# Kernel optimization log

Measured on AMD Instinct MI355X. Metric: run time of the kernel, lower is better.

## Reference

```python
import jax, jax.numpy as jnp
import numpy as np

DIM = 4096
R = 128
B, S = 4, 4096


def setup_inputs() -> dict:
    key = jax.random.key(0)
    k1, k2, k3 = jax.random.split(key, 3)
    x = jax.random.normal(k1, (B, S, DIM), dtype=jnp.float32)
    # PyTorch Linear default init: U(-1/sqrt(fan_in), 1/sqrt(fan_in)); approx with scaled normal
    W_down = jax.random.normal(k2, (R, DIM), dtype=jnp.float32) * (1.0 / np.sqrt(DIM))
    W_up = jax.random.normal(k3, (DIM, R), dtype=jnp.float32) * (1.0 / np.sqrt(R))
    return {"x": x, "W_down": W_down, "W_up": W_up}


def reference(x, W_down, W_up):
    # RMSNorm (no learned scale, eps = finfo(dtype).eps as in F.rms_norm default)
    eps = jnp.finfo(x.dtype).eps
    ms = jnp.mean(jnp.square(x), axis=-1, keepdims=True)
    xn = x * jax.lax.rsqrt(ms + eps)
    # low-rank gate: sigmoid(W_up @ silu(W_down @ xn))
    h = jax.nn.silu(jnp.einsum('bsd,rd->bsr', xn, W_down))  # [B,S,R]
    gate = jax.nn.sigmoid(jnp.einsum('bsr,dr->bsd', h, W_up))  # [B,S,DIM]
    return xn * gate
```

## Files before the change

kernel.cpp:

```cpp
#include <hip/hip_runtime.h>
#include <hip/hip_bf16.h>


#define DIMX  4096
#define RLOW  128
#define BT    16
#define THREADS 256

typedef __attribute__((ext_vector_type(8))) short  bf16x8;
typedef __attribute__((ext_vector_type(4))) float  f32x4;

__device__ __forceinline__ unsigned short f2bf(float f) {
    unsigned int u = __float_as_uint(f);
    u = u + 0x7fffu + ((u >> 16) & 1u);
    return (unsigned short)(u >> 16);
}
__device__ __forceinline__ float bf2f(unsigned short s) {
    return __uint_as_float((unsigned int)s << 16);
}
__device__ __forceinline__ float sigm(float v) { return 1.0f / (1.0f + __expf(-v)); }

__device__ __forceinline__ void cvt8_store(unsigned short* dst, float4 a, float4 b) {
    ushort4 u0, u1;
    u0.x = f2bf(a.x); u0.y = f2bf(a.y); u0.z = f2bf(a.z); u0.w = f2bf(a.w);
    u1.x = f2bf(b.x); u1.y = f2bf(b.y); u1.z = f2bf(b.z); u1.w = f2bf(b.w);
    *(ushort4*)dst = u0;
    *(ushort4*)(dst + 4) = u1;
}

__global__ __launch_bounds__(THREADS)
void prep_weights_frag(const float* __restrict__ wd, const float* __restrict__ wu,
                       unsigned short* __restrict__ wd_frag,
                       unsigned short* __restrict__ wu_frag) {
    const int tg = blockIdx.x * THREADS + threadIdx.x;
    if (tg < 65536) {
        const int frag = tg >> 6, lane = tg & 63;
        const int wave = frag & 3, nt = (frag >> 2) & 1, ks = (frag >> 3) & 7, c = frag >> 6;
        const int r = wave * 32 + nt * 16 + (lane & 15);
        const int k = c * 256 + ks * 32 + 8 * (lane >> 4);
        const float* src = wd + (long)r * DIMX + k;
        cvt8_store(wd_frag + ((long)frag << 9) + lane * 8,
                   *(const float4*)src, *(const float4*)(src + 4));
    } else {
        const int t2 = tg - 65536;
        const int frag = t2 >> 6, lane = t2 & 63;
        const int d_tile = frag >> 2, ks = frag & 3;
        const int row = d_tile * 16 + (lane & 15);
        const int col = ks * 32 + 8 * (lane >> 4);
        const float* src = wu + (long)row * RLOW + col;
        cvt8_store(wu_frag + ((long)frag << 9) + lane * 8,
                   *(const float4*)src, *(const float4*)(src + 4));
    }
}

#define KC        256
#define NCH       (DIMX / KC)
#define XB_STRIDE 8192
#define INV1_OFF  (2 * XB_STRIDE)
#define LDS1_BYTES (INV1_OFF + BT * 4)

__global__ __launch_bounds__(THREADS, 6)
void down_kernel(const float* __restrict__ x,
                 const unsigned short* __restrict__ wd_frag,
                 unsigned short* __restrict__ h_ws,
                 float* __restrict__ invr_ws) {
    extern __shared__ char smem[];
    const int tid  = threadIdx.x;
    const int lane = tid & 63;
    const int wave = tid >> 6;
    const int l15  = lane & 15;
    const int lq   = lane >> 4;

    const long tok0 = (long)blockIdx.x * BT;
    const float* __restrict__ xblk = x + tok0 * DIMX;

    const int srow = tid >> 4;
    const int su   = tid & 15;

    float ss = 0.f;
    float4 v[4];

    {
        const float4* src = (const float4*)(xblk + (long)srow * DIMX);
        #pragma unroll
        for (int j = 0; j < 4; ++j) v[j] = src[su + 16 * j];
        #pragma unroll
        for (int j = 0; j < 4; ++j) {
            float4 f = v[j];
            ss += f.x * f.x + f.y * f.y + f.z * f.z + f.w * f.w;
            ushort4 u4;
            u4.x = f2bf(f.x); u4.y = f2bf(f.y); u4.z = f2bf(f.z); u4.w = f2bf(f.w);
            int byte = (srow * 512 + 8 * (su + 16 * j)) ^ ((srow & 7) << 4);
            *(ushort4*)(smem + byte) = u4;
        }
    }
    __syncthreads();

    f32x4 hacc[2] = {{0.f, 0.f, 0.f, 0.f}, {0.f, 0.f, 0.f, 0.f}};

    for (int c = 0; c < NCH; ++c) {
        if (c + 1 < NCH) {
            const float4* src = (const float4*)(xblk + (long)srow * DIMX + (c + 1) * KC);
            #pragma unroll
            for (int j = 0; j < 4; ++j) v[j] = src[su + 16 * j];
        }
        const char* xbuf = smem + (c & 1) * XB_STRIDE;
        const unsigned short* fb = wd_frag + (((long)c * 8 * 2 * 4) << 9) + lane * 8;
        #pragma unroll
        for (int ks = 0; ks < KC / 32; ++ks) {
            const int kk = ks * 32 + 8 * lq;
            const int abyte = (l15 * 512 + kk * 2) ^ ((l15 & 7) << 4);
            bf16x8 a = *(const bf16x8*)(xbuf + abyte);
            #pragma unroll
            for (int nt = 0; nt < 2; ++nt) {
                bf16x8 b = *(const bf16x8*)(fb + ((long)((ks * 2 + nt) * 4 + wave) << 9));
                hacc[nt] = __builtin_amdgcn_mfma_f32_16x16x32_bf16(a, b, hacc[nt], 0, 0, 0);
            }
        }
        if (c + 1 < NCH) {
            char* nbuf = smem + ((c + 1) & 1) * XB_STRIDE;
            #pragma unroll
            for (int j = 0; j < 4; ++j) {
                float4 f = v[j];
                ss += f.x * f.x + f.y * f.y + f.z * f.z + f.w * f.w;
                ushort4 u4;
                u4.x = f2bf(f.x); u4.y = f2bf(f.y); u4.z = f2bf(f.z); u4.w = f2bf(f.w);
                int byte = (srow * 512 + 8 * (su + 16 * j)) ^ ((srow & 7) << 4);
                *(ushort4*)(nbuf + byte) = u4;
            }
        }
        __syncthreads();
    }

    #pragma unroll
    for (int m = 1; m < 16; m <<= 1) ss += __shfl_xor(ss, m, 64);
    if (su == 0) {
        float invr = rsqrtf(ss * (1.0f / DIMX) + 1.1920929e-07f);
        *(float*)(smem + INV1_OFF + srow * 4) = invr;
        invr_ws[tok0 + srow] = invr;
    }
    __syncthreads();

    const int n0w = wave * 32;
    #pragma unroll
    for (int nt = 0; nt < 2; ++nt) {
        const int r = n0w + nt * 16 + l15;
        #pragma unroll
        for (int i = 0; i < 4; ++i) {
            const int t = 4 * lq + i;
            float invr = *(const float*)(smem + INV1_OFF + t * 4);
            float hp = hacc[nt][i] * invr;
            float hs = hp * sigm(hp);
            h_ws[(tok0 + t) * RLOW + r] = f2bf(hs);
        }
    }
}

#define SLAB_US   2176
#define UP_LDS_BYTES (4 * SLAB_US * 2)

__global__ __launch_bounds__(THREADS, 6)
void up_kernel(const float* __restrict__ x,
               const unsigned short* __restrict__ wu_frag,
               const unsigned short* __restrict__ h_ws,
               const float* __restrict__ invr_ws,
               float* __restrict__ out) {
    extern __shared__ char smem[];
    const int tid  = threadIdx.x;
    const int lane = tid & 63;
    const int wave = tid >> 6;
    const int l15  = lane & 15;
    const int lq   = lane >> 4;

    const int tb   = blockIdx.x >> 2;
    const int dblk = blockIdx.x & 3;
    const long tok0 = (long)tb * BT;

    bf16x8 hb[4];
    #pragma unroll
    for (int ks = 0; ks < 4; ++ks)
        hb[ks] = *(const bf16x8*)(h_ws + (tok0 + l15) * RLOW + ks * 32 + 8 * lq);
    const float invr_t = invr_ws[tok0 + l15];

    unsigned short* slab = (unsigned short*)smem + wave * SLAB_US;

    #pragma unroll
    for (int sg = 0; sg < 2; ++sg) {
        const int colbase = dblk * 1024 + wave * 256 + sg * 128;
        const int dt0 = colbase >> 4;

        #pragma unroll
        for (int tg = 0; tg < 8; ++tg) {
            bf16x8 wa[4];
            #pragma unroll
            for (int ks = 0; ks < 4; ++ks)
                wa[ks] = *(const bf16x8*)(wu_frag + ((long)((dt0 + tg) * 4 + ks) << 9) + lane * 8);
            f32x4 acc = {0.f, 0.f, 0.f, 0.f};
            #pragma unroll
            for (int ks = 0; ks < 4; ++ks)
                acc = __builtin_amdgcn_mfma_f32_16x16x32_bf16(wa[ks], hb[ks], acc, 0, 0, 0);
            ushort4 g4;
            g4.x = f2bf(sigm(acc[0]) * invr_t);
            g4.y = f2bf(sigm(acc[1]) * invr_t);
            g4.z = f2bf(sigm(acc[2]) * invr_t);
            g4.w = f2bf(sigm(acc[3]) * invr_t);
            *(ushort4*)(slab + l15 * 136 + tg * 16 + lq * 4) = g4;
        }
        const int token_lo = lane >> 5;
        const int cw = (lane & 31) * 4;
        float4  xf[8];
        ushort4 gv[8];
        #pragma unroll
        for (int it = 0; it < 8; ++it) {
            const int token = 2 * it + token_lo;
            xf[it] = *(const float4*)(x + (tok0 + token) * DIMX + colbase + cw);
        }
        #pragma unroll
        for (int it = 0; it < 8; ++it) {
            const int token = 2 * it + token_lo;
            gv[it] = *(const ushort4*)(slab + token * 136 + cw);
        }
        #pragma unroll
        for (int it = 0; it < 8; ++it) {
            const int token = 2 * it + token_lo;
            float4 o;
            o.x = xf[it].x * bf2f(gv[it].x);
            o.y = xf[it].y * bf2f(gv[it].y);
            o.z = xf[it].z * bf2f(gv[it].z);
            o.w = xf[it].w * bf2f(gv[it].w);
            *(float4*)(out + (tok0 + token) * DIMX + colbase + cw) = o;
        }
    }
}

#define FKC   512
#define FNCH  (DIMX / FKC)
#define FXB_STRIDE 16384
#define HP        136
#define H_OFF     (2 * FXB_STRIDE)
#define INV_OFF   (H_OFF + BT * HP * 2)
#define LDSF_BYTES (INV_OFF + BT * 4)

__device__ __forceinline__ bf16x8 load_w8_f32(const float* __restrict__ wf, long off) {
    float4 a = *(const float4*)(wf + off);
    float4 b = *(const float4*)(wf + off + 4);
    bf16x8 r;
    r[0] = (short)f2bf(a.x); r[1] = (short)f2bf(a.y);
    r[2] = (short)f2bf(a.z); r[3] = (short)f2bf(a.w);
    r[4] = (short)f2bf(b.x); r[5] = (short)f2bf(b.y);
    r[6] = (short)f2bf(b.z); r[7] = (short)f2bf(b.w);
    return r;
}

__global__ __launch_bounds__(THREADS)
void fused_fallback(const float* __restrict__ x,
                    const float* __restrict__ wd_f32,
                    const float* __restrict__ wu_f32,
                    float* __restrict__ out) {
    extern __shared__ char smem[];
    const int tid  = threadIdx.x;
    const int lane = tid & 63;
    const int wave = tid >> 6;
    const int l15  = lane & 15;
    const int lq   = lane >> 4;
    const long tok0 = (long)blockIdx.x * BT;
    const float* __restrict__ xblk = x + tok0 * DIMX;
    float* __restrict__ outblk = out + tok0 * DIMX;
    const int srow = tid >> 4;
    const int su   = tid & 15;
    float ss = 0.f;
    float4 v[8];
    {
        const float4* src = (const float4*)(xblk + (long)srow * DIMX);
        #pragma unroll
        for (int j = 0; j < 8; ++j) v[j] = src[su + 16 * j];
        #pragma unroll
        for (int j = 0; j < 8; ++j) {
            float4 f = v[j];
            ss += f.x * f.x + f.y * f.y + f.z * f.z + f.w * f.w;
            ushort4 u4;
            u4.x = f2bf(f.x); u4.y = f2bf(f.y); u4.z = f2bf(f.z); u4.w = f2bf(f.w);
            int byte = (srow * 1024 + 8 * (su + 16 * j)) ^ ((srow & 7) << 4);
            *(ushort4*)(smem + byte) = u4;
        }
    }
    __syncthreads();
    f32x4 hacc[2] = {{0.f, 0.f, 0.f, 0.f}, {0.f, 0.f, 0.f, 0.f}};
    const int n0w = wave * 32;
    for (int c = 0; c < FNCH; ++c) {
        if (c + 1 < FNCH) {
            const float4* src = (const float4*)(xblk + (long)srow * DIMX + (c + 1) * FKC);
            #pragma unroll
            for (int j = 0; j < 8; ++j) v[j] = src[su + 16 * j];
        }
        const char* xbuf = smem + (c & 1) * FXB_STRIDE;
        #pragma unroll 4
        for (int ks = 0; ks < FKC / 32; ++ks) {
            const int kk = ks * 32 + 8 * lq;
            const int abyte = (l15 * 1024 + kk * 2) ^ ((l15 & 7) << 4);
            bf16x8 a = *(const bf16x8*)(xbuf + abyte);
            const long kg = (long)c * FKC + kk;
            #pragma unroll
            for (int nt = 0; nt < 2; ++nt) {
                const int r = n0w + nt * 16 + l15;
                bf16x8 b = load_w8_f32(wd_f32, (long)r * DIMX + kg);
                hacc[nt] = __builtin_amdgcn_mfma_f32_16x16x32_bf16(a, b, hacc[nt], 0, 0, 0);
            }
        }
        if (c + 1 < FNCH) {
            char* nbuf = smem + ((c + 1) & 1) * FXB_STRIDE;
            #pragma unroll
            for (int j = 0; j < 8; ++j) {
                float4 f = v[j];
                ss += f.x * f.x + f.y * f.y + f.z * f.z + f.w * f.w;
                ushort4 u4;
                u4.x = f2bf(f.x); u4.y = f2bf(f.y); u4.z = f2bf(f.z); u4.w = f2bf(f.w);
                int byte = (srow * 1024 + 8 * (su + 16 * j)) ^ ((srow & 7) << 4);
                *(ushort4*)(nbuf + byte) = u4;
            }
        }
        __syncthreads();
    }
    #pragma unroll
    for (int m = 1; m < 16; m <<= 1) ss += __shfl_xor(ss, m, 64);
    if (su == 0) {
        float invr = rsqrtf(ss * (1.0f / DIMX) + 1.1920929e-07f);
        *(float*)(smem + INV_OFF + srow * 4) = invr;
    }
    __syncthreads();
    #pragma unroll
    for (int nt = 0; nt < 2; ++nt) {
        const int r = n0w + nt * 16 + l15;
        #pragma unroll
        for (int i = 0; i < 4; ++i) {
            const int t = 4 * lq + i;
            float invr = *(const float*)(smem + INV_OFF + t * 4);
            float hp = hacc[nt][i] * invr;
            float hs = hp * sigm(hp);
            *(unsigned short*)(smem + H_OFF + (t * HP + r) * 2) = f2bf(hs);
        }
    }
    __syncthreads();
    bf16x8 hb[4];
    #pragma unroll
    for (int ks = 0; ks < 4; ++ks)
        hb[ks] = *(const bf16x8*)(smem + H_OFF + (l15 * HP + ks * 32 + 8 * lq) * 2);
    const float invr_t = *(const float*)(smem + INV_OFF + l15 * 4);
    const int t = l15;
    const int wbase = wave * (DIMX / 4);
    for (int g = 0; g < 16; ++g) {
        const int d0 = wbase + g * 64;
        bf16x8 wa[4][4];
        #pragma unroll
        for (int tt = 0; tt < 4; ++tt) {
            const int drow = d0 + tt * 16 + l15;
            #pragma unroll
            for (int ks = 0; ks < 4; ++ks)
                wa[tt][ks] = load_w8_f32(wu_f32, (long)drow * RLOW + ks * 32 + 8 * lq);
        }
        f32x4 acc[4] = {{0.f,0.f,0.f,0.f},{0.f,0.f,0.f,0.f},{0.f,0.f,0.f,0.f},{0.f,0.f,0.f,0.f}};
        #pragma unroll
        for (int ks = 0; ks < 4; ++ks)
            #pragma unroll
            for (int tt = 0; tt < 4; ++tt)
                acc[tt] = __builtin_amdgcn_mfma_f32_16x16x32_bf16(wa[tt][ks], hb[ks], acc[tt], 0, 0, 0);
        #pragma unroll
        for (int tt = 0; tt < 4; ++tt) {
            const int dc = d0 + tt * 16 + 4 * lq;
            float4 xf = *(const float4*)(xblk + (long)t * DIMX + dc);
            float4 o;
            o.x = xf.x * invr_t * sigm(acc[tt][0]);
            o.y = xf.y * invr_t * sigm(acc[tt][1]);
            o.z = xf.z * invr_t * sigm(acc[tt][2]);
            o.w = xf.w * invr_t * sigm(acc[tt][3]);
            *(float4*)(outblk + (long)t * DIMX + dc) = o;
        }
    }
}

extern "C" void kernel_launch(void* const* d_in, const int* in_sizes, int n_in,
                              void* d_out, int out_size, void* d_ws, size_t ws_size,
                              hipStream_t stream) {
    const float* x  = (const float*)d_in[0];
    const float* wd = (const float*)d_in[1];
    const float* wu = (const float*)d_in[2];
    float* out = (float*)d_out;

    const int ntok = in_sizes[0] / DIMX;
    const int nblk = ntok / BT;

    const size_t need = (size_t)2 * RLOW * DIMX * 2
                      + (size_t)ntok * RLOW * 2
                      + (size_t)ntok * 4;
    if (ws_size >= need) {
        unsigned short* wd_frag = (unsigned short*)d_ws;
        unsigned short* wu_frag = wd_frag + (size_t)RLOW * DIMX;
        unsigned short* h_ws    = wu_frag + (size_t)RLOW * DIMX;
        float*          invr_ws = (float*)(h_ws + (size_t)ntok * RLOW);
        prep_weights_frag<<<512, THREADS, 0, stream>>>(wd, wu, wd_frag, wu_frag);
        down_kernel<<<nblk, THREADS, LDS1_BYTES, stream>>>(x, wd_frag, h_ws, invr_ws);
        up_kernel<<<nblk * 4, THREADS, UP_LDS_BYTES, stream>>>(x, wu_frag, h_ws, invr_ws, out);
    } else {
        fused_fallback<<<nblk, THREADS, LDSF_BYTES, stream>>>(x, wd, wu, out);
    }
}
```

Baseline: 212.7 us.

## Widen down_kernel to 512 threads with one MFMA column tile per wave

The down projection kernel now runs 512 threads (8 waves) per block instead of 256. Each wave owns a single 16-wide rank tile rather than two, and each thread streams half as many float4s of x per chunk. The goal is more memory-level parallelism and latency hiding when loading x. The launch bounds for up_kernel are also raised from 6 to 7 blocks per CU, which may raise occupancy but tightens the register budget.

```diff
diff --git a/kernel.cpp b/kernel.cpp
--- a/kernel.cpp
+++ b/kernel.cpp
@@ -6,6 +6,7 @@
 #define RLOW  128
 #define BT    16
 #define THREADS 256
+#define DTHREADS 512
 
 typedef __attribute__((ext_vector_type(8))) short  bf16x8;
 typedef __attribute__((ext_vector_type(4))) float  f32x4;
@@ -59,7 +60,7 @@
 #define INV1_OFF  (2 * XB_STRIDE)
 #define LDS1_BYTES (INV1_OFF + BT * 4)
 
-__global__ __launch_bounds__(THREADS, 6)
+__global__ __launch_bounds__(DTHREADS, 8)
 void down_kernel(const float* __restrict__ x,
                  const unsigned short* __restrict__ wd_frag,
                  unsigned short* __restrict__ h_ws,
@@ -74,58 +75,56 @@
     const long tok0 = (long)blockIdx.x * BT;
     const float* __restrict__ xblk = x + tok0 * DIMX;
 
-    const int srow = tid >> 4;
-    const int su   = tid & 15;
+    const int srow = tid >> 5;
+    const int su   = tid & 31;
 
     float ss = 0.f;
-    float4 v[4];
+    float4 v[2];
 
     {
         const float4* src = (const float4*)(xblk + (long)srow * DIMX);
-        #pragma unroll
-        for (int j = 0; j < 4; ++j) v[j] = src[su + 16 * j];
-        #pragma unroll
-        for (int j = 0; j < 4; ++j) {
+        v[0] = src[su];
+        v[1] = src[su + 32];
+        #pragma unroll
+        for (int j = 0; j < 2; ++j) {
             float4 f = v[j];
             ss += f.x * f.x + f.y * f.y + f.z * f.z + f.w * f.w;
             ushort4 u4;
             u4.x = f2bf(f.x); u4.y = f2bf(f.y); u4.z = f2bf(f.z); u4.w = f2bf(f.w);
-            int byte = (srow * 512 + 8 * (su + 16 * j)) ^ ((srow & 7) << 4);
+            int byte = (srow * 512 + 8 * (su + 32 * j)) ^ ((srow & 7) << 4);
             *(ushort4*)(smem + byte) = u4;
         }
     }
     __syncthreads();
 
-    f32x4 hacc[2] = {{0.f, 0.f, 0.f, 0.f}, {0.f, 0.f, 0.f, 0.f}};
+    f32x4 hacc = {0.f, 0.f, 0.f, 0.f};
+    const int fw = (wave & 1) * 4 + (wave >> 1);
 
     for (int c = 0; c < NCH; ++c) {
         if (c + 1 < NCH) {
             const float4* src = (const float4*)(xblk + (long)srow * DIMX + (c + 1) * KC);
-            #pragma unroll
-            for (int j = 0; j < 4; ++j) v[j] = src[su + 16 * j];
+            v[0] = src[su];
+            v[1] = src[su + 32];
         }
         const char* xbuf = smem + (c & 1) * XB_STRIDE;
-        const unsigned short* fb = wd_frag + (((long)c * 8 * 2 * 4) << 9) + lane * 8;
-        #pragma unroll
-        for (int ks = 0; ks < KC / 32; ++ks) {
+        const unsigned short* fb = wd_frag + (((long)c * 64) << 9) + lane * 8;
+        #pragma unroll
+        for (int ks = 0; ks < 8; ++ks) {
             const int kk = ks * 32 + 8 * lq;
             const int abyte = (l15 * 512 + kk * 2) ^ ((l15 & 7) << 4);
             bf16x8 a = *(const bf16x8*)(xbuf + abyte);
-            #pragma unroll
-            for (int nt = 0; nt < 2; ++nt) {
-                bf16x8 b = *(const bf16x8*)(fb + ((long)((ks * 2 + nt) * 4 + wave) << 9));
-                hacc[nt] = __builtin_amdgcn_mfma_f32_16x16x32_bf16(a, b, hacc[nt], 0, 0, 0);
-            }
+            bf16x8 b = *(const bf16x8*)(fb + ((long)(ks * 8 + fw) << 9));
+            hacc = __builtin_amdgcn_mfma_f32_16x16x32_bf16(a, b, hacc, 0, 0, 0);
         }
         if (c + 1 < NCH) {
             char* nbuf = smem + ((c + 1) & 1) * XB_STRIDE;
             #pragma unroll
-            for (int j = 0; j < 4; ++j) {
+            for (int j = 0; j < 2; ++j) {
                 float4 f = v[j];
                 ss += f.x * f.x + f.y * f.y + f.z * f.z + f.w * f.w;
                 ushort4 u4;
                 u4.x = f2bf(f.x); u4.y = f2bf(f.y); u4.z = f2bf(f.z); u4.w = f2bf(f.w);
-                int byte = (srow * 512 + 8 * (su + 16 * j)) ^ ((srow & 7) << 4);
+                int byte = (srow * 512 + 8 * (su + 32 * j)) ^ ((srow & 7) << 4);
                 *(ushort4*)(nbuf + byte) = u4;
             }
         }
@@ -133,7 +132,7 @@
     }
 
     #pragma unroll
-    for (int m = 1; m < 16; m <<= 1) ss += __shfl_xor(ss, m, 64);
+    for (int m = 1; m < 32; m <<= 1) ss += __shfl_xor(ss, m, 64);
     if (su == 0) {
         float invr = rsqrtf(ss * (1.0f / DIMX) + 1.1920929e-07f);
         *(float*)(smem + INV1_OFF + srow * 4) = invr;
@@ -141,25 +140,21 @@
     }
     __syncthreads();
 
-    const int n0w = wave * 32;
-    #pragma unroll
-    for (int nt = 0; nt < 2; ++nt) {
-        const int r = n0w + nt * 16 + l15;
-        #pragma unroll
-        for (int i = 0; i < 4; ++i) {
-            const int t = 4 * lq + i;
-            float invr = *(const float*)(smem + INV1_OFF + t * 4);
-            float hp = hacc[nt][i] * invr;
-            float hs = hp * sigm(hp);
-            h_ws[(tok0 + t) * RLOW + r] = f2bf(hs);
-        }
+    const int r = wave * 16 + l15;
+    #pragma unroll
+    for (int i = 0; i < 4; ++i) {
+        const int t = 4 * lq + i;
+        float invr = *(const float*)(smem + INV1_OFF + t * 4);
+        float hp = hacc[i] * invr;
+        float hs = hp * sigm(hp);
+        h_ws[(tok0 + t) * RLOW + r] = f2bf(hs);
     }
 }
 
 #define SLAB_US   2176
 #define UP_LDS_BYTES (4 * SLAB_US * 2)
 
-__global__ __launch_bounds__(THREADS, 6)
+__global__ __launch_bounds__(THREADS, 7)
 void up_kernel(const float* __restrict__ x,
                const unsigned short* __restrict__ wu_frag,
                const unsigned short* __restrict__ h_ws,
@@ -398,7 +393,7 @@
         unsigned short* h_ws    = wu_frag + (size_t)RLOW * DIMX;
         float*          invr_ws = (float*)(h_ws + (size_t)ntok * RLOW);
         prep_weights_frag<<<512, THREADS, 0, stream>>>(wd, wu, wd_frag, wu_frag);
-        down_kernel<<<nblk, THREADS, LDS1_BYTES, stream>>>(x, wd_frag, h_ws, invr_ws);
+        down_kernel<<<nblk, DTHREADS, LDS1_BYTES, stream>>>(x, wd_frag, h_ws, invr_ws);
         up_kernel<<<nblk * 4, THREADS, UP_LDS_BYTES, stream>>>(x, wu_frag, h_ws, invr_ws, out);
     } else {
         fused_fallback<<<nblk, THREADS, LDSF_BYTES, stream>>>(x, wd, wu, out);
```

Result: slower. 277.9 us (+30.6%).
